# Performance work log

Hardware: AMD Instinct MI355X
Metric: run time of the kernel (lower is better)

Reference implementation:

```python
import jax, jax.numpy as jnp
import numpy as np

H = 128          # hidden_dim
L = 3            # n_layers
G = 128          # num graphs in batch
BN_EPS = 1e-5


def setup_inputs() -> dict:
    key = jax.random.key(0)
    ks = jax.random.split(key, 16)
    N, E, ND, ED = 2048, 8192, 32, 16
    s = lambda k, shape, fan: jax.random.normal(k, shape, dtype=jnp.float32) / np.sqrt(fan)
    return {
        "x": jax.random.normal(ks[0], (N, ND), dtype=jnp.float32),
        "edge_index": jax.random.randint(ks[1], (2, E), 0, N),
        "edge_attr": jax.random.normal(ks[2], (E, ED), dtype=jnp.float32),
        "batch": jnp.sort(jax.random.randint(ks[3], (N,), 0, G)),
        "node_W": s(ks[4], (ND, H), ND),
        "node_b": jnp.zeros((H,), jnp.float32),
        "edge_W": s(ks[5], (L, ED, H * H), ED),
        "edge_b": jnp.zeros((L, H * H), jnp.float32),
        "root_W": s(ks[6], (L, H, H), H),
        "conv_bias": jnp.zeros((L, H), jnp.float32),
        "bn_gamma": jnp.ones((L, H), jnp.float32),
        "bn_beta": jnp.zeros((L, H), jnp.float32),
        "cls_W1": s(ks[7], (H, 64), H),
        "cls_b1": jnp.zeros((64,), jnp.float32),
        "cls_W2": s(ks[8], (64, 1), 64),
        "cls_b2": jnp.zeros((1,), jnp.float32),
    }


def _segment_mean(vals, ids, num_segments):
    ssum = jax.ops.segment_sum(vals, ids, num_segments=num_segments)
    cnt = jax.ops.segment_sum(jnp.ones((vals.shape[0],), vals.dtype), ids,
                              num_segments=num_segments)
    return ssum / jnp.maximum(cnt, 1.0)[:, None]


def reference(x, edge_index, edge_attr, batch, node_W, node_b, edge_W, edge_b,
              root_W, conv_bias, bn_gamma, bn_beta, cls_W1, cls_b1, cls_W2, cls_b2):
    N = x.shape[0]
    src, dst = edge_index[0], edge_index[1]
    h = x @ node_W + node_b                                   # [N, H]
    for l in range(L):
        # edge-conditioned weights: [E, H, H]
        W = (edge_attr @ edge_W[l] + edge_b[l]).reshape(-1, H, H)
        msg = jnp.einsum('ei,eio->eo', h[src], W)             # gather + per-edge matmul
        agg = _segment_mean(msg, dst, N)                      # scatter-mean
        x_new = h @ root_W[l] + agg + conv_bias[l]
        # BatchNorm (batch statistics, training-mode math)
        mu = jnp.mean(x_new, axis=0)
        var = jnp.var(x_new, axis=0)
        x_new = (x_new - mu) * jax.lax.rsqrt(var + BN_EPS) * bn_gamma[l] + bn_beta[l]
        x_new = jax.nn.relu(x_new)                            # dropout omitted (eval)
        h = h + x_new                                         # residual
    g = _segment_mean(h, batch, G)                            # global mean pool [G, H]
    out = jax.nn.relu(g @ cls_W1 + cls_b1) @ cls_W2 + cls_b2  # classifier
    return out.squeeze(-1)                                    # [G]
```

## Files before the change

### kernel.cpp

```cpp
#include <hip/hip_runtime.h>
#include <cstddef>
#include <cstdint>

#define H 128
#define EDIM 16
#define NLAYER 3
#define KU 2304
#define NSLICE 18

typedef unsigned short ushort_t;
typedef unsigned int uint_t;
typedef __attribute__((ext_vector_type(8))) short bf16x8;
typedef __attribute__((ext_vector_type(4))) float f32x4;

__device__ __forceinline__ ushort_t f2bf(float f) {
    uint_t u = __builtin_bit_cast(uint_t, f);
    u += 0x7fffu + ((u >> 16) & 1u);
    return (ushort_t)(u >> 16);
}
__device__ __forceinline__ uint_t pack2(float a, float b) {
    return (uint_t)f2bf(a) | ((uint_t)f2bf(b) << 16);
}

__global__ __launch_bounds__(256) void setup_kernel(
    const int* __restrict__ dst, const int* __restrict__ batch,
    const float* __restrict__ x, const float* __restrict__ node_W,
    const float* __restrict__ node_b,
    const float* __restrict__ eW, const float* __restrict__ eb,
    const float* __restrict__ rW,
    int* __restrict__ offs, int* __restrict__ deg, int* __restrict__ eord,
    float* __restrict__ cntG, float* __restrict__ bnS, float* __restrict__ bnQ,
    float* __restrict__ gsum, float* __restrict__ h, ushort_t* __restrict__ Wt2,
    int E, int N, int G)
{
    alignas(16) __shared__ unsigned char smem[34816];
    const int b = blockIdx.x;
    const int t = threadIdx.x;
    const int NBe = (N / 64) * 2;

    if (b == 0) {
        int* sh = (int*)smem;
        int* part = sh + 2048;
        for (int i = t; i < N; i += 256) sh[i] = 0;
        __syncthreads();
        for (int e = t; e < E; e += 256) atomicAdd(&sh[dst[e]], 1);
        __syncthreads();
        const int base = t * 8;
        int v[8], loc[8], s = 0;
#pragma unroll
        for (int j = 0; j < 8; ++j) v[j] = (base + j < N) ? sh[base + j] : 0;
#pragma unroll
        for (int j = 0; j < 8; ++j) { loc[j] = s; s += v[j]; }
        part[t] = s;
        __syncthreads();
        for (int off = 1; off < 256; off <<= 1) {
            int xp = (t >= off) ? part[t - off] : 0;
            __syncthreads();
            part[t] += xp;
            __syncthreads();
        }
        const int boff = (t == 0) ? 0 : part[t - 1];
#pragma unroll
        for (int j = 0; j < 8; ++j) {
            if (base + j < N) {
                deg[base + j] = v[j];
                offs[base + j] = boff + loc[j];
            }
        }
        if (t == 255) offs[N] = boff + s;
        __syncthreads();
        for (int i = t; i < N; i += 256) sh[i] = offs[i];
        __syncthreads();
        for (int e = t; e < E; e += 256) {
            const int d = dst[e];
            const int pos = atomicAdd(&sh[d], 1);
            eord[pos] = e;
        }
        return;
    }

    if (b <= NLAYER * NSLICE) {
        ushort_t* tile = (ushort_t*)smem;
        const int bb = b - 1;
        const int l = bb / NSLICE, s = bb % NSLICE;
        const float* S = (s < 16) ? (eW + ((size_t)l * 16 + s) * (H * H))
                       : (s == 16 ? (eb + (size_t)l * H * H)
                                  : (rW + (size_t)l * H * H));
        const int k = t >> 1, o0 = (t & 1) * 64;
#pragma unroll
        for (int j = 0; j < 64; j += 4) {
            float4 v = *(const float4*)&S[(size_t)k * H + o0 + j];
            tile[k * 136 + o0 + j + 0] = f2bf(v.x);
            tile[k * 136 + o0 + j + 1] = f2bf(v.y);
            tile[k * 136 + o0 + j + 2] = f2bf(v.z);
            tile[k * 136 + o0 + j + 3] = f2bf(v.w);
        }
        __syncthreads();
        const int n = t >> 1, k0 = (t & 1) * 64;
        ushort_t* outp = Wt2 + ((size_t)(l * H + n)) * KU + s * H + k0;
#pragma unroll 8
        for (int j = 0; j < 64; ++j) outp[j] = tile[(k0 + j) * 136 + n];
        return;
    }

    if (b <= NLAYER * NSLICE + NBe) {
        float* As = (float*)smem;
        float* Bs = As + 16 * 68;
        const int tt = b - (NLAYER * NSLICE + 1);
        const int bm = (tt >> 1) * 64;
        const int bn = (tt & 1) * 64;
        const int tx = t & 15, ty = t >> 4;
        float acc[4][4];
#pragma unroll
        for (int i = 0; i < 4; ++i)
#pragma unroll
            for (int j = 0; j < 4; ++j) acc[i][j] = 0.f;
        const int ka = t & 15, ma = t >> 4;
        const int nb = t & 63, kb = t >> 6;
        for (int k0 = 0; k0 < 32; k0 += 16) {
#pragma unroll
            for (int r = 0; r < 4; ++r)
                As[ka * 68 + ma + 16 * r] = x[(size_t)(bm + ma + 16 * r) * 32 + (k0 + ka)];
#pragma unroll
            for (int r = 0; r < 4; ++r)
                Bs[(kb + 4 * r) * 68 + nb] = node_W[(size_t)(k0 + kb + 4 * r) * H + bn + nb];
            __syncthreads();
#pragma unroll
            for (int kk = 0; kk < 16; ++kk) {
                const float4 a4 = *(const float4*)&As[kk * 68 + ty * 4];
                const float4 b4 = *(const float4*)&Bs[kk * 68 + tx * 4];
                const float a[4] = {a4.x, a4.y, a4.z, a4.w};
                const float bv[4] = {b4.x, b4.y, b4.z, b4.w};
#pragma unroll
                for (int i = 0; i < 4; ++i)
#pragma unroll
                    for (int j = 0; j < 4; ++j)
                        acc[i][j] = fmaf(a[i], bv[j], acc[i][j]);
            }
            __syncthreads();
        }
#pragma unroll
        for (int i = 0; i < 4; ++i) {
            const int row = bm + ty * 4 + i;
            float4 v;
            v.x = acc[i][0] + node_b[bn + tx * 4 + 0];
            v.y = acc[i][1] + node_b[bn + tx * 4 + 1];
            v.z = acc[i][2] + node_b[bn + tx * 4 + 2];
            v.w = acc[i][3] + node_b[bn + tx * 4 + 3];
            *(float4*)&h[(size_t)row * H + bn + tx * 4] = v;
        }
        return;
    }

    {
        const int zcount = G * H + 2 * NLAYER * H + G;
        for (int i = t; i < zcount; i += 256) {
            if (i < G * H) gsum[i] = 0.f;
            else if (i < G * H + NLAYER * H) bnS[i - G * H] = 0.f;
            else if (i < G * H + 2 * NLAYER * H) bnQ[i - G * H - NLAYER * H] = 0.f;
            else cntG[i - G * H - 2 * NLAYER * H] = 0.f;
        }
        __syncthreads();
        for (int v = t; v < N; v += 256) atomicAdd(&cntG[batch[v]], 1.f);
    }
}

__global__ __launch_bounds__(256) void ubuild_kernel(
    const float* __restrict__ h, const float* __restrict__ ea,
    const int* __restrict__ src, const int* __restrict__ offs,
    const int* __restrict__ deg, const int* __restrict__ eord,
    ushort_t* __restrict__ Ub, int N)
{
    const int tid = threadIdx.x;
    const int sb = tid >> 6;
    const int j = tid & 63;
    const int v = blockIdx.x * 4 + sb;
    if (v >= N) return;

    float u[17][2];
#pragma unroll
    for (int d = 0; d < 17; ++d) { u[d][0] = 0.f; u[d][1] = 0.f; }

    const int st = offs[v];
    const int dg = deg[v];
    for (int k = 0; k < dg; ++k) {
        const int e = eord[st + k];
        const int s = src[e];
        const float* eap = ea + (size_t)e * EDIM;
        const float4 w0 = *(const float4*)(eap + 0);
        const float4 w1 = *(const float4*)(eap + 4);
        const float4 w2 = *(const float4*)(eap + 8);
        const float4 w3 = *(const float4*)(eap + 12);
        const float w[16] = {w0.x, w0.y, w0.z, w0.w, w1.x, w1.y, w1.z, w1.w,
                             w2.x, w2.y, w2.z, w2.w, w3.x, w3.y, w3.z, w3.w};
        const float2 h2 = *(const float2*)&h[(size_t)s * H + 2 * j];
        u[16][0] += h2.x;
        u[16][1] += h2.y;
#pragma unroll
        for (int d = 0; d < 16; ++d) {
            u[d][0] = fmaf(w[d], h2.x, u[d][0]);
            u[d][1] = fmaf(w[d], h2.y, u[d][1]);
        }
    }
    const float rc = 1.0f / (float)(dg > 0 ? dg : 1);
    uint_t* outp = (uint_t*)(Ub + (size_t)v * KU) + j;
#pragma unroll
    for (int d = 0; d < 17; ++d)
        outp[(size_t)d * 64] = pack2(u[d][0] * rc, u[d][1] * rc);
    const float2 hv = *(const float2*)&h[(size_t)v * H + 2 * j];
    outp[(size_t)17 * 64] = pack2(hv.x, hv.y);
}

__global__ __launch_bounds__(256) void gemm_stats(
    const ushort_t* __restrict__ Ub, const ushort_t* __restrict__ Wt2l,
    float* __restrict__ xnew, float* __restrict__ bnS, float* __restrict__ bnQ)
{
    __shared__ ushort_t As[16][136];
    __shared__ ushort_t Bs[128][136];
    const int tid = threadIdx.x;
    const int m0 = blockIdx.x * 16;
    const int wave = tid >> 6, lane = tid & 63;
    const int l15 = lane & 15, quad = lane >> 4;

    f32x4 acc0 = {0.f, 0.f, 0.f, 0.f};
    f32x4 acc1 = {0.f, 0.f, 0.f, 0.f};

    for (int c = 0; c < KU / 128; ++c) {
        {
            const int row = tid >> 4, pos = (tid & 15) * 8;
            *(uint4*)&As[row][pos] =
                *(const uint4*)&Ub[(size_t)(m0 + row) * KU + c * 128 + pos];
        }
#pragma unroll
        for (int r = 0; r < 8; ++r) {
            const int idx = tid + r * 256;
            const int row = idx >> 4, pos = (idx & 15) * 8;
            *(uint4*)&Bs[row][pos] =
                *(const uint4*)&Wt2l[(size_t)row * KU + c * 128 + pos];
        }
        __syncthreads();
#pragma unroll
        for (int ks = 0; ks < 4; ++ks) {
            const int k = ks * 32 + quad * 8;
            bf16x8 a  = *(const bf16x8*)&As[l15][k];
            bf16x8 b0 = *(const bf16x8*)&Bs[wave * 16 + l15][k];
            bf16x8 b1 = *(const bf16x8*)&Bs[(wave + 4) * 16 + l15][k];
            acc0 = __builtin_amdgcn_mfma_f32_16x16x32_bf16(a, b0, acc0, 0, 0, 0);
            acc1 = __builtin_amdgcn_mfma_f32_16x16x32_bf16(a, b1, acc1, 0, 0, 0);
        }
        __syncthreads();
    }

    float s0 = 0.f, q0 = 0.f, s1 = 0.f, q1 = 0.f;
#pragma unroll
    for (int r = 0; r < 4; ++r) {
        const int row = m0 + quad * 4 + r;
        const float v0 = acc0[r];
        const float v1 = acc1[r];
        xnew[(size_t)row * H + wave * 16 + l15] = v0;
        xnew[(size_t)row * H + (wave + 4) * 16 + l15] = v1;
        s0 += v0; q0 += v0 * v0;
        s1 += v1; q1 += v1 * v1;
    }
    s0 += __shfl_down(s0, 32); s0 += __shfl_down(s0, 16);
    q0 += __shfl_down(q0, 32); q0 += __shfl_down(q0, 16);
    s1 += __shfl_down(s1, 32); s1 += __shfl_down(s1, 16);
    q1 += __shfl_down(q1, 32); q1 += __shfl_down(q1, 16);
    if (quad == 0) {
        atomicAdd(&bnS[wave * 16 + l15], s0);
        atomicAdd(&bnQ[wave * 16 + l15], q0);
        atomicAdd(&bnS[(wave + 4) * 16 + l15], s1);
        atomicAdd(&bnQ[(wave + 4) * 16 + l15], q1);
    }
}

__global__ __launch_bounds__(256) void bn_apply(
    float* __restrict__ h, const float* __restrict__ xnew,
    const float* __restrict__ bnS, const float* __restrict__ bnQ,
    const float* __restrict__ gamma, const float* __restrict__ beta,
    const int* __restrict__ batch, float* __restrict__ gsum, int N, int last)
{
    const int idx = blockIdx.x * 256 + threadIdx.x;
    const int c = idx & 127;
    const int v = idx >> 7;
    const float invN = 1.0f / (float)N;
    const float mu = bnS[c] * invN;
    const float var = bnQ[c] * invN - mu * mu;
    const float val = (xnew[idx] - mu) * rsqrtf(var + 1e-5f) * gamma[c] + beta[c];
    const float hn = h[idx] + fmaxf(val, 0.f);
    h[idx] = hn;
    if (last) atomicAdd(&gsum[batch[v] * H + c], hn);
}

__global__ void classifier_kernel(
    const float* __restrict__ gsum, const float* __restrict__ cntG,
    const float* __restrict__ W1, const float* __restrict__ b1,
    const float* __restrict__ W2, const float* __restrict__ b2,
    float* __restrict__ out)
{
    const int g = blockIdx.x;
    const int j = threadIdx.x;
    const float rc = 1.0f / fmaxf(cntG[g], 1.0f);
    float acc = b1[j];
#pragma unroll 8
    for (int i = 0; i < H; ++i)
        acc = fmaf(gsum[g * H + i] * rc, W1[i * 64 + j], acc);
    float pv = fmaxf(acc, 0.f) * W2[j];
#pragma unroll
    for (int off = 32; off > 0; off >>= 1)
        pv += __shfl_down(pv, off);
    if (j == 0) out[g] = pv + b2[0];
}

extern "C" void kernel_launch(void* const* d_in, const int* in_sizes, int n_in,
                              void* d_out, int out_size, void* d_ws, size_t ws_size,
                              hipStream_t stream)
{
    const float* x      = (const float*)d_in[0];
    const int*   eidx   = (const int*)  d_in[1];
    const float* eattr  = (const float*)d_in[2];
    const int*   batch  = (const int*)  d_in[3];
    const float* node_W = (const float*)d_in[4];
    const float* node_b = (const float*)d_in[5];
    const float* edge_W = (const float*)d_in[6];
    const float* edge_b = (const float*)d_in[7];
    const float* root_W = (const float*)d_in[8];
    const float* gamma  = (const float*)d_in[10];
    const float* beta   = (const float*)d_in[11];
    const float* W1     = (const float*)d_in[12];
    const float* b1     = (const float*)d_in[13];
    const float* W2     = (const float*)d_in[14];
    const float* b2     = (const float*)d_in[15];
    float* out = (float*)d_out;

    const int N = in_sizes[0] / 32;
    const int E = in_sizes[1] / 2;
    const int G = out_size;

    const int* src = eidx;
    const int* dst = eidx + E;

    int* offs  = (int*)d_ws;
    int* deg   = offs + (N + 16);
    int* eord  = deg + N;
    float* cntG = (float*)(eord + E);
    float* bnS  = cntG + G;
    float* bnQ  = bnS + NLAYER * H;
    float* gsum = bnQ + NLAYER * H;
    float* h    = gsum + (size_t)G * H;
    float* xnew = h + (size_t)N * H;
    ushort_t* Wt2 = (ushort_t*)(xnew + (size_t)N * H);
    ushort_t* Ub  = Wt2 + (size_t)NLAYER * H * KU;

    const int NBe = (N / 64) * 2;
    const int nsetup = 1 + NLAYER * NSLICE + NBe + 1;

    setup_kernel<<<nsetup, 256, 0, stream>>>(
        dst, batch, x, node_W, node_b, edge_W, edge_b, root_W,
        offs, deg, eord, cntG, bnS, bnQ, gsum, h, Wt2, E, N, G);

    for (int l = 0; l < NLAYER; ++l) {
        ubuild_kernel<<<N / 4, 256, 0, stream>>>(
            h, eattr, src, offs, deg, eord, Ub, N);
        gemm_stats<<<N / 16, 256, 0, stream>>>(
            Ub, Wt2 + (size_t)l * H * KU, xnew, bnS + l * H, bnQ + l * H);
        bn_apply<<<(N * H) / 256, 256, 0, stream>>>(
            h, xnew, bnS + l * H, bnQ + l * H,
            gamma + (size_t)l * H, beta + (size_t)l * H,
            batch, gsum, N, l == NLAYER - 1);
    }

    classifier_kernel<<<G, 64, 0, stream>>>(gsum, cntG, W1, b1, W2, b2, out);
}
```

Measured before the change: 224.9 us.

## Fuse per-node U build into GEMM kernel and widen setup blocks to 1024 threads

Merges the per-node aggregation kernel that built the bf16 U matrix with the MFMA GEMM. Each 512-thread block builds eight rows of U directly in shared memory and then multiplies them against the layer weights, so U is never written to or read back from global memory and one launch per layer disappears. The setup kernel now runs 1024-thread blocks, with fewer, wider blocks for the CSR scan, weight transpose and node-embedding GEMM. In exchange, the MFMA tile now uses only 8 real rows of its 16-row A operand, half of each MFMA is wasted, and the full weight matrix is streamed from memory for every 8 rows instead of every 16.

```diff
diff --git a/kernel.cpp b/kernel.cpp
--- a/kernel.cpp
+++ b/kernel.cpp
@@ -7,6 +7,7 @@
 #define NLAYER 3
 #define KU 2304
 #define NSLICE 18
+#define ASTRIDE 2312
 
 typedef unsigned short ushort_t;
 typedef unsigned int uint_t;
@@ -22,7 +23,7 @@
     return (uint_t)f2bf(a) | ((uint_t)f2bf(b) << 16);
 }
 
-__global__ __launch_bounds__(256) void setup_kernel(
+__global__ __launch_bounds__(1024) void setup_kernel(
     const int* __restrict__ dst, const int* __restrict__ batch,
     const float* __restrict__ x, const float* __restrict__ node_W,
     const float* __restrict__ node_b,
@@ -33,45 +34,36 @@
     float* __restrict__ gsum, float* __restrict__ h, ushort_t* __restrict__ Wt2,
     int E, int N, int G)
 {
-    alignas(16) __shared__ unsigned char smem[34816];
+    alignas(16) __shared__ unsigned char smem[36864];
     const int b = blockIdx.x;
     const int t = threadIdx.x;
-    const int NBe = (N / 64) * 2;
 
     if (b == 0) {
         int* sh = (int*)smem;
         int* part = sh + 2048;
-        for (int i = t; i < N; i += 256) sh[i] = 0;
-        __syncthreads();
-        for (int e = t; e < E; e += 256) atomicAdd(&sh[dst[e]], 1);
-        __syncthreads();
-        const int base = t * 8;
-        int v[8], loc[8], s = 0;
-#pragma unroll
-        for (int j = 0; j < 8; ++j) v[j] = (base + j < N) ? sh[base + j] : 0;
-#pragma unroll
-        for (int j = 0; j < 8; ++j) { loc[j] = s; s += v[j]; }
-        part[t] = s;
-        __syncthreads();
-        for (int off = 1; off < 256; off <<= 1) {
+        for (int i = t; i < N; i += 1024) sh[i] = 0;
+        __syncthreads();
+        for (int e = t; e < E; e += 1024) atomicAdd(&sh[dst[e]], 1);
+        __syncthreads();
+        const int v0 = (2 * t < N) ? sh[2 * t] : 0;
+        const int v1 = (2 * t + 1 < N) ? sh[2 * t + 1] : 0;
+        part[t] = v0 + v1;
+        __syncthreads();
+        for (int off = 1; off < 1024; off <<= 1) {
             int xp = (t >= off) ? part[t - off] : 0;
             __syncthreads();
             part[t] += xp;
             __syncthreads();
         }
         const int boff = (t == 0) ? 0 : part[t - 1];
-#pragma unroll
-        for (int j = 0; j < 8; ++j) {
-            if (base + j < N) {
-                deg[base + j] = v[j];
-                offs[base + j] = boff + loc[j];
-            }
-        }
-        if (t == 255) offs[N] = boff + s;
-        __syncthreads();
-        for (int i = t; i < N; i += 256) sh[i] = offs[i];
-        __syncthreads();
-        for (int e = t; e < E; e += 256) {
+        if (2 * t < N) { deg[2 * t] = v0; offs[2 * t] = boff; }
+        if (2 * t + 1 < N) { deg[2 * t + 1] = v1; offs[2 * t + 1] = boff + v0; }
+        if (t == 1023) offs[N] = part[1023];
+        __syncthreads();
+        if (2 * t < N) sh[2 * t] = boff;
+        if (2 * t + 1 < N) sh[2 * t + 1] = boff + v0;
+        __syncthreads();
+        for (int e = t; e < E; e += 1024) {
             const int d = dst[e];
             const int pos = atomicAdd(&sh[d], 1);
             eord[pos] = e;
@@ -86,9 +78,9 @@
         const float* S = (s < 16) ? (eW + ((size_t)l * 16 + s) * (H * H))
                        : (s == 16 ? (eb + (size_t)l * H * H)
                                   : (rW + (size_t)l * H * H));
-        const int k = t >> 1, o0 = (t & 1) * 64;
-#pragma unroll
-        for (int j = 0; j < 64; j += 4) {
+        const int k = t >> 3, o0 = (t & 7) * 16;
+#pragma unroll
+        for (int j = 0; j < 16; j += 4) {
             float4 v = *(const float4*)&S[(size_t)k * H + o0 + j];
             tile[k * 136 + o0 + j + 0] = f2bf(v.x);
             tile[k * 136 + o0 + j + 1] = f2bf(v.y);
@@ -96,27 +88,29 @@
             tile[k * 136 + o0 + j + 3] = f2bf(v.w);
         }
         __syncthreads();
-        const int n = t >> 1, k0 = (t & 1) * 64;
+        const int n = t >> 3, k0 = (t & 7) * 16;
         ushort_t* outp = Wt2 + ((size_t)(l * H + n)) * KU + s * H + k0;
-#pragma unroll 8
-        for (int j = 0; j < 64; ++j) outp[j] = tile[(k0 + j) * 136 + n];
+#pragma unroll
+        for (int j = 0; j < 16; ++j) outp[j] = tile[(k0 + j) * 136 + n];
         return;
     }
 
-    if (b <= NLAYER * NSLICE + NBe) {
-        float* As = (float*)smem;
+    if (b <= NLAYER * NSLICE + 16) {
+        const int sub = t >> 8;
+        const int st = t & 255;
+        float* As = (float*)(smem + sub * 8704);
         float* Bs = As + 16 * 68;
-        const int tt = b - (NLAYER * NSLICE + 1);
+        const int tt = (b - (NLAYER * NSLICE + 1)) * 4 + sub;
         const int bm = (tt >> 1) * 64;
         const int bn = (tt & 1) * 64;
-        const int tx = t & 15, ty = t >> 4;
+        const int tx = st & 15, ty = st >> 4;
         float acc[4][4];
 #pragma unroll
         for (int i = 0; i < 4; ++i)
 #pragma unroll
             for (int j = 0; j < 4; ++j) acc[i][j] = 0.f;
-        const int ka = t & 15, ma = t >> 4;
-        const int nb = t & 63, kb = t >> 6;
+        const int ka = st & 15, ma = st >> 4;
+        const int nb = st & 63, kb = st >> 6;
         for (int k0 = 0; k0 < 32; k0 += 16) {
 #pragma unroll
             for (int r = 0; r < 4; ++r)
@@ -154,86 +148,75 @@
 
     {
         const int zcount = G * H + 2 * NLAYER * H + G;
-        for (int i = t; i < zcount; i += 256) {
+        for (int i = t; i < zcount; i += 1024) {
             if (i < G * H) gsum[i] = 0.f;
             else if (i < G * H + NLAYER * H) bnS[i - G * H] = 0.f;
             else if (i < G * H + 2 * NLAYER * H) bnQ[i - G * H - NLAYER * H] = 0.f;
             else cntG[i - G * H - 2 * NLAYER * H] = 0.f;
         }
         __syncthreads();
-        for (int v = t; v < N; v += 256) atomicAdd(&cntG[batch[v]], 1.f);
-    }
-}
-
-__global__ __launch_bounds__(256) void ubuild_kernel(
+        for (int v = t; v < N; v += 1024) atomicAdd(&cntG[batch[v]], 1.f);
+    }
+}
+
+__global__ __launch_bounds__(512, 4) void ubuild_gemm(
     const float* __restrict__ h, const float* __restrict__ ea,
     const int* __restrict__ src, const int* __restrict__ offs,
     const int* __restrict__ deg, const int* __restrict__ eord,
-    ushort_t* __restrict__ Ub, int N)
-{
-    const int tid = threadIdx.x;
-    const int sb = tid >> 6;
-    const int j = tid & 63;
-    const int v = blockIdx.x * 4 + sb;
-    if (v >= N) return;
-
-    float u[17][2];
-#pragma unroll
-    for (int d = 0; d < 17; ++d) { u[d][0] = 0.f; u[d][1] = 0.f; }
-
-    const int st = offs[v];
-    const int dg = deg[v];
-    for (int k = 0; k < dg; ++k) {
-        const int e = eord[st + k];
-        const int s = src[e];
-        const float* eap = ea + (size_t)e * EDIM;
-        const float4 w0 = *(const float4*)(eap + 0);
-        const float4 w1 = *(const float4*)(eap + 4);
-        const float4 w2 = *(const float4*)(eap + 8);
-        const float4 w3 = *(const float4*)(eap + 12);
-        const float w[16] = {w0.x, w0.y, w0.z, w0.w, w1.x, w1.y, w1.z, w1.w,
-                             w2.x, w2.y, w2.z, w2.w, w3.x, w3.y, w3.z, w3.w};
-        const float2 h2 = *(const float2*)&h[(size_t)s * H + 2 * j];
-        u[16][0] += h2.x;
-        u[16][1] += h2.y;
-#pragma unroll
-        for (int d = 0; d < 16; ++d) {
-            u[d][0] = fmaf(w[d], h2.x, u[d][0]);
-            u[d][1] = fmaf(w[d], h2.y, u[d][1]);
-        }
-    }
-    const float rc = 1.0f / (float)(dg > 0 ? dg : 1);
-    uint_t* outp = (uint_t*)(Ub + (size_t)v * KU) + j;
-#pragma unroll
-    for (int d = 0; d < 17; ++d)
-        outp[(size_t)d * 64] = pack2(u[d][0] * rc, u[d][1] * rc);
-    const float2 hv = *(const float2*)&h[(size_t)v * H + 2 * j];
-    outp[(size_t)17 * 64] = pack2(hv.x, hv.y);
-}
-
-__global__ __launch_bounds__(256) void gemm_stats(
-    const ushort_t* __restrict__ Ub, const ushort_t* __restrict__ Wt2l,
+    const ushort_t* __restrict__ Wt2l,
     float* __restrict__ xnew, float* __restrict__ bnS, float* __restrict__ bnQ)
 {
-    __shared__ ushort_t As[16][136];
+    __shared__ ushort_t As8[8 * ASTRIDE];
     __shared__ ushort_t Bs[128][136];
     const int tid = threadIdx.x;
-    const int m0 = blockIdx.x * 16;
-    const int wave = tid >> 6, lane = tid & 63;
+    const int w = tid >> 6;
+    const int lane = tid & 63;
+    const int m0 = blockIdx.x * 8;
+
+    {
+        const int v = m0 + w;
+        const int j = lane;
+        float u[17][2];
+#pragma unroll
+        for (int d = 0; d < 17; ++d) { u[d][0] = 0.f; u[d][1] = 0.f; }
+        const int st = offs[v];
+        const int dg = deg[v];
+        for (int k = 0; k < dg; ++k) {
+            const int e = eord[st + k];
+            const int s = src[e];
+            const float* eap = ea + (size_t)e * EDIM;
+            const float4 w0 = *(const float4*)(eap + 0);
+            const float4 w1 = *(const float4*)(eap + 4);
+            const float4 w2 = *(const float4*)(eap + 8);
+            const float4 w3 = *(const float4*)(eap + 12);
+            const float wv[16] = {w0.x, w0.y, w0.z, w0.w, w1.x, w1.y, w1.z, w1.w,
+                                  w2.x, w2.y, w2.z, w2.w, w3.x, w3.y, w3.z, w3.w};
+            const float2 h2 = *(const float2*)&h[(size_t)s * H + 2 * j];
+            u[16][0] += h2.x;
+            u[16][1] += h2.y;
+#pragma unroll
+            for (int d = 0; d < 16; ++d) {
+                u[d][0] = fmaf(wv[d], h2.x, u[d][0]);
+                u[d][1] = fmaf(wv[d], h2.y, u[d][1]);
+            }
+        }
+        const float rc = 1.0f / (float)(dg > 0 ? dg : 1);
+        uint_t* urow = (uint_t*)&As8[w * ASTRIDE];
+#pragma unroll
+        for (int d = 0; d < 17; ++d)
+            urow[j + d * 64] = pack2(u[d][0] * rc, u[d][1] * rc);
+        const float2 hv = *(const float2*)&h[(size_t)v * H + 2 * j];
+        urow[j + 17 * 64] = pack2(hv.x, hv.y);
+    }
+
     const int l15 = lane & 15, quad = lane >> 4;
-
-    f32x4 acc0 = {0.f, 0.f, 0.f, 0.f};
-    f32x4 acc1 = {0.f, 0.f, 0.f, 0.f};
+    f32x4 acc = {0.f, 0.f, 0.f, 0.f};
+    const ushort_t* arow = &As8[(l15 & 7) * ASTRIDE];
 
     for (int c = 0; c < KU / 128; ++c) {
-        {
-            const int row = tid >> 4, pos = (tid & 15) * 8;
-            *(uint4*)&As[row][pos] =
-                *(const uint4*)&Ub[(size_t)(m0 + row) * KU + c * 128 + pos];
-        }
-#pragma unroll
-        for (int r = 0; r < 8; ++r) {
-            const int idx = tid + r * 256;
+#pragma unroll
+        for (int r = 0; r < 4; ++r) {
+            const int idx = tid + r * 512;
             const int row = idx >> 4, pos = (idx & 15) * 8;
             *(uint4*)&Bs[row][pos] =
                 *(const uint4*)&Wt2l[(size_t)row * KU + c * 128 + pos];
@@ -242,35 +225,30 @@
 #pragma unroll
         for (int ks = 0; ks < 4; ++ks) {
             const int k = ks * 32 + quad * 8;
-            bf16x8 a  = *(const bf16x8*)&As[l15][k];
-            bf16x8 b0 = *(const bf16x8*)&Bs[wave * 16 + l15][k];
-            bf16x8 b1 = *(const bf16x8*)&Bs[(wave + 4) * 16 + l15][k];
-            acc0 = __builtin_amdgcn_mfma_f32_16x16x32_bf16(a, b0, acc0, 0, 0, 0);
-            acc1 = __builtin_amdgcn_mfma_f32_16x16x32_bf16(a, b1, acc1, 0, 0, 0);
-        }
-        __syncthreads();
-    }
-
-    float s0 = 0.f, q0 = 0.f, s1 = 0.f, q1 = 0.f;
-#pragma unroll
-    for (int r = 0; r < 4; ++r) {
-        const int row = m0 + quad * 4 + r;
-        const float v0 = acc0[r];
-        const float v1 = acc1[r];
-        xnew[(size_t)row * H + wave * 16 + l15] = v0;
-        xnew[(size_t)row * H + (wave + 4) * 16 + l15] = v1;
-        s0 += v0; q0 += v0 * v0;
-        s1 += v1; q1 += v1 * v1;
-    }
-    s0 += __shfl_down(s0, 32); s0 += __shfl_down(s0, 16);
-    q0 += __shfl_down(q0, 32); q0 += __shfl_down(q0, 16);
-    s1 += __shfl_down(s1, 32); s1 += __shfl_down(s1, 16);
-    q1 += __shfl_down(q1, 32); q1 += __shfl_down(q1, 16);
-    if (quad == 0) {
-        atomicAdd(&bnS[wave * 16 + l15], s0);
-        atomicAdd(&bnQ[wave * 16 + l15], q0);
-        atomicAdd(&bnS[(wave + 4) * 16 + l15], s1);
-        atomicAdd(&bnQ[(wave + 4) * 16 + l15], q1);
+            bf16x8 a = *(const bf16x8*)&arow[c * 128 + k];
+            bf16x8 b = *(const bf16x8*)&Bs[w * 16 + l15][k];
+            acc = __builtin_amdgcn_mfma_f32_16x16x32_bf16(a, b, acc, 0, 0, 0);
+        }
+        __syncthreads();
+    }
+
+    const int col = w * 16 + l15;
+    float s = 0.f, q = 0.f;
+    if (quad < 2) {
+#pragma unroll
+        for (int r = 0; r < 4; ++r) {
+            const int m = quad * 4 + r;
+            const float val = acc[r];
+            xnew[(size_t)(m0 + m) * H + col] = val;
+            s += val;
+            q += val * val;
+        }
+    }
+    s += __shfl_down(s, 16);
+    q += __shfl_down(q, 16);
+    if (lane < 16) {
+        atomicAdd(&bnS[col], s);
+        atomicAdd(&bnQ[col], q);
     }
 }
 
@@ -350,20 +328,18 @@
     float* h    = gsum + (size_t)G * H;
     float* xnew = h + (size_t)N * H;
     ushort_t* Wt2 = (ushort_t*)(xnew + (size_t)N * H);
-    ushort_t* Ub  = Wt2 + (size_t)NLAYER * H * KU;
-
-    const int NBe = (N / 64) * 2;
-    const int nsetup = 1 + NLAYER * NSLICE + NBe + 1;
-
-    setup_kernel<<<nsetup, 256, 0, stream>>>(
+
+    const int nsetup = 1 + NLAYER * NSLICE + 16 + 1;
+
+    setup_kernel<<<nsetup, 1024, 0, stream>>>(
         dst, batch, x, node_W, node_b, edge_W, edge_b, root_W,
         offs, deg, eord, cntG, bnS, bnQ, gsum, h, Wt2, E, N, G);
 
     for (int l = 0; l < NLAYER; ++l) {
-        ubuild_kernel<<<N / 4, 256, 0, stream>>>(
-            h, eattr, src, offs, deg, eord, Ub, N);
-        gemm_stats<<<N / 16, 256, 0, stream>>>(
-            Ub, Wt2 + (size_t)l * H * KU, xnew, bnS + l * H, bnQ + l * H);
+        ubuild_gemm<<<N / 8, 512, 0, stream>>>(
+            h, eattr, src, offs, deg, eord,
+            Wt2 + (size_t)l * H * KU,
+            xnew, bnS + l * H, bnQ + l * H);
         bn_apply<<<(N * H) / 256, 256, 0, stream>>>(
             h, xnew, bnS + l * H, bnQ + l * H,
             gamma + (size_t)l * H, beta + (size_t)l * H,
```

Result: faster. 206.5 us (-8.2%).
